# Kernel tuning notes

Hardware: AMD Instinct MI355X
Metric: run time of the kernel (lower is better)

## Reference

```python
import jax, jax.numpy as jnp
import numpy as np

K = 3          # kernel_size
G = 8          # groups
R = 4          # channel reduction ratio
D = 1          # dilation
M = D * (K - 1)
M2 = M // 2


def setup_inputs() -> dict:
    key = jax.random.key(0)
    ks = jax.random.split(key, 5)
    B, C, Hin, Win = 8, 128, 130, 130
    Cr = C // R
    x = jax.random.normal(ks[0], (B, C, Hin, Win), jnp.float32)
    W_reduce = jax.random.normal(ks[1], (Cr, C), jnp.float32) / np.float32(np.sqrt(C))
    b_reduce = jax.random.normal(ks[2], (Cr,), jnp.float32) * 0.01
    W_kern = jax.random.normal(ks[3], (G * K * K, Cr), jnp.float32) / np.float32(np.sqrt(Cr))
    b_kern = jax.random.normal(ks[4], (G * K * K,), jnp.float32) * 0.01
    return dict(x=x, W_reduce=W_reduce, b_reduce=b_reduce, W_kern=W_kern, b_kern=b_kern)


def reference(x, W_reduce, b_reduce, W_kern, b_kern):
    B, C, Hin, Win = x.shape
    H, W = Hin - M, Win - M            # stride=1, padding=0
    CG = C // G
    # unfold (im2col), torch ordering: channel outer, kernel-position inner
    patches = jnp.stack(
        [x[:, :, i * D:i * D + H, j * D:j * D + W] for i in range(K) for j in range(K)],
        axis=2,
    )                                   # [B, C, K2, H, W]
    patches = patches.reshape(B, G, CG, K * K, H, W)
    # center crop for kernel generation (pool is Identity since stride=1)
    xc = x[:, :, M2:Hin - M2, M2:Win - M2]            # [B, C, H, W]
    red = jnp.einsum('rc,bchw->brhw', W_reduce, xc) + b_reduce[None, :, None, None]
    kern = jnp.einsum('or,brhw->bohw', W_kern, red) + b_kern[None, :, None, None]
    kern = kern.reshape(B, G, K * K, H, W)
    # per-pixel dynamic kernel multiply-sum over K2
    out = jnp.einsum('bgkhw,bgckhw->bgchw', kern, patches)
    return out.reshape(B, C, H, W)
```

## Files before the change

kernel.cpp:

```cpp
#include <hip/hip_runtime.h>

namespace {
constexpr int HIN = 130, WIN = 130;
constexpr int HH = 128, WW = 128;
constexpr int C = 128, CR = 32, B = 8;
constexpr int CHW = HIN * WIN;

__global__ void transpose_wred(const float* __restrict__ Wred, float* __restrict__ WredT) {
    int idx = blockIdx.x * 256 + threadIdx.x;
    int r = idx >> 7;
    int c = idx & 127;
    WredT[c * CR + r] = Wred[r * C + c];
}

__device__ __forceinline__ void lgkm_barrier() {
    asm volatile("s_waitcnt lgkmcnt(0)\n\ts_barrier" ::: "memory");
    __builtin_amdgcn_sched_barrier(0);
}

__global__ __launch_bounds__(256, 4) void invol_direct(
    const float* __restrict__ x,
    const float* __restrict__ WredT,
    const float* __restrict__ bred,
    const float* __restrict__ Wkern,
    const float* __restrict__ bkern,
    float* __restrict__ out)
{
    __shared__ float red2[CR][128];

    const int t = threadIdx.x;
    const int p = t & 63;
    const int q = __builtin_amdgcn_readfirstlane(t >> 6);

    const int orig = blockIdx.x;
    const int blk  = (orig & 7) * 128 + (orig >> 3);
    const int b    = blk >> 7;
    const int h    = blk & (HH - 1);

    const float* xb = x + (size_t)b * C * CHW;

    const float* xc = xb + (size_t)(h + 1) * WIN + (2 * p + 1);
    float r0[8], r1[8];
#pragma unroll
    for (int r = 0; r < 8; ++r) { r0[r] = bred[q * 8 + r]; r1[r] = r0[r]; }

#pragma unroll
    for (int cb = 0; cb < 4; ++cb) {
        float xv0[32], xv1[32];
#pragma unroll
        for (int cc = 0; cc < 32; ++cc) {
            const float* cp = xc + (size_t)(cb * 32 + cc) * CHW;
            xv0[cc] = cp[0];
            xv1[cc] = cp[1];
        }
#pragma unroll
        for (int cc = 0; cc < 32; ++cc) {
#pragma unroll
            for (int r = 0; r < 8; ++r) {
                float wgt = WredT[(cb * 32 + cc) * CR + q * 8 + r];
                r0[r] = fmaf(wgt, xv0[cc], r0[r]);
                r1[r] = fmaf(wgt, xv1[cc], r1[r]);
            }
        }
    }
#pragma unroll
    for (int r = 0; r < 8; ++r)
        *(float2*)&red2[q * 8 + r][2 * p] = make_float2(r0[r], r1[r]);

    lgkm_barrier();

    float k0[18], k1[18];
#pragma unroll
    for (int k = 0; k < 18; ++k) { k0[k] = bkern[18 * q + k]; k1[k] = k0[k]; }
#pragma unroll
    for (int r = 0; r < CR; ++r) {
        float2 rv = *(const float2*)&red2[r][2 * p];
#pragma unroll
        for (int k = 0; k < 18; ++k) {
            float wgt = Wkern[(18 * q + k) * CR + r];
            k0[k] = fmaf(wgt, rv.x, k0[k]);
            k1[k] = fmaf(wgt, rv.y, k1[k]);
        }
    }

    const float* xrow = xb + (size_t)h * WIN + 2 * p;
    float* op = out + (((size_t)(b * C + 32 * q)) * HH + h) * WW + 2 * p;

#pragma unroll
    for (int half = 0; half < 2; ++half) {
        float kh0[9], kh1[9];
#pragma unroll
        for (int k = 0; k < 9; ++k) { kh0[k] = k0[9 * half + k]; kh1[k] = k1[9 * half + k]; }

#pragma unroll 2
        for (int cc = 0; cc < 16; ++cc) {
            const float* xp = xrow + (size_t)(32 * q + 16 * half + cc) * CHW;
            float2 ta[3], tb[3];
#pragma unroll
            for (int i = 0; i < 3; ++i) {
                ta[i] = *(const float2*)(xp + i * WIN);
                tb[i] = *(const float2*)(xp + i * WIN + 2);
            }
            float a0 = 0.f, a1 = 0.f;
#pragma unroll
            for (int i = 0; i < 3; ++i) {
                a0 = fmaf(kh0[3 * i + 0], ta[i].x, a0);
                a0 = fmaf(kh0[3 * i + 1], ta[i].y, a0);
                a0 = fmaf(kh0[3 * i + 2], tb[i].x, a0);
                a1 = fmaf(kh1[3 * i + 0], ta[i].y, a1);
                a1 = fmaf(kh1[3 * i + 1], tb[i].x, a1);
                a1 = fmaf(kh1[3 * i + 2], tb[i].y, a1);
            }
            *(float2*)(op + (size_t)(16 * half + cc) * HH * WW) = make_float2(a0, a1);
        }
    }
}
}

extern "C" void kernel_launch(void* const* d_in, const int* in_sizes, int n_in,
                              void* d_out, int out_size, void* d_ws, size_t ws_size,
                              hipStream_t stream) {
    const float* x     = (const float*)d_in[0];
    const float* Wred  = (const float*)d_in[1];
    const float* bred  = (const float*)d_in[2];
    const float* Wkern = (const float*)d_in[3];
    const float* bkern = (const float*)d_in[4];
    float* out   = (float*)d_out;
    float* WredT = (float*)d_ws;

    transpose_wred<<<16, 256, 0, stream>>>(Wred, WredT);

    invol_direct<<<1024, 256, 0, stream>>>(x, WredT, bred, Wkern, bkern, out);
}
```

Measured before the change: 58.59 us.

## Software-pipeline channel loads with double buffers and compute kernel weights per half

Splits the channel-reduction loads into 16-channel chunks held in two register buffers, so the next chunk's global loads are issued before the FMAs on the current chunk. The output stage now prefetches the 3x3 patches of the next four channels while computing the current four. The first patch load is issued before the barrier. Kernel weights are generated one half (9 taps) at a time, interleaved with the output loop, which lowers the live register count. The risk is extra VGPR pressure from the 48 float2 patch buffers, which could hurt occupancy under launch_bounds(256,4) or cause spills.

```diff
diff --git a/kernel.cpp b/kernel.cpp
--- a/kernel.cpp
+++ b/kernel.cpp
@@ -44,76 +44,106 @@
 #pragma unroll
     for (int r = 0; r < 8; ++r) { r0[r] = bred[q * 8 + r]; r1[r] = r0[r]; }
 
+    float A0[16], A1[16], B0[16], B1[16];
+
+    auto ld1 = [&](float (&v0)[16], float (&v1)[16], int cb) {
 #pragma unroll
-    for (int cb = 0; cb < 4; ++cb) {
-        float xv0[32], xv1[32];
+        for (int cc = 0; cc < 16; ++cc) {
+            const float* cp = xc + (size_t)(cb * 16 + cc) * CHW;
+            v0[cc] = cp[0];
+            v1[cc] = cp[1];
+        }
+    };
+    auto fma1 = [&](const float (&v0)[16], const float (&v1)[16], int cb) {
 #pragma unroll
-        for (int cc = 0; cc < 32; ++cc) {
-            const float* cp = xc + (size_t)(cb * 32 + cc) * CHW;
-            xv0[cc] = cp[0];
-            xv1[cc] = cp[1];
-        }
-#pragma unroll
-        for (int cc = 0; cc < 32; ++cc) {
+        for (int cc = 0; cc < 16; ++cc) {
 #pragma unroll
             for (int r = 0; r < 8; ++r) {
-                float wgt = WredT[(cb * 32 + cc) * CR + q * 8 + r];
-                r0[r] = fmaf(wgt, xv0[cc], r0[r]);
-                r1[r] = fmaf(wgt, xv1[cc], r1[r]);
+                float wgt = WredT[(cb * 16 + cc) * CR + q * 8 + r];
+                r0[r] = fmaf(wgt, v0[cc], r0[r]);
+                r1[r] = fmaf(wgt, v1[cc], r1[r]);
             }
+        }
+    };
+
+    ld1(A0, A1, 0);
+#pragma unroll
+    for (int cb = 0; cb < 8; ++cb) {
+        if ((cb & 1) == 0) {
+            if (cb < 7) ld1(B0, B1, cb + 1);
+            fma1(A0, A1, cb);
+        } else {
+            if (cb < 7) ld1(A0, A1, cb + 1);
+            fma1(B0, B1, cb);
         }
     }
 #pragma unroll
     for (int r = 0; r < 8; ++r)
         *(float2*)&red2[q * 8 + r][2 * p] = make_float2(r0[r], r1[r]);
 
-    lgkm_barrier();
-
-    float k0[18], k1[18];
-#pragma unroll
-    for (int k = 0; k < 18; ++k) { k0[k] = bkern[18 * q + k]; k1[k] = k0[k]; }
-#pragma unroll
-    for (int r = 0; r < CR; ++r) {
-        float2 rv = *(const float2*)&red2[r][2 * p];
-#pragma unroll
-        for (int k = 0; k < 18; ++k) {
-            float wgt = Wkern[(18 * q + k) * CR + r];
-            k0[k] = fmaf(wgt, rv.x, k0[k]);
-            k1[k] = fmaf(wgt, rv.y, k1[k]);
-        }
-    }
-
     const float* xrow = xb + (size_t)h * WIN + 2 * p;
     float* op = out + (((size_t)(b * C + 32 * q)) * HH + h) * WW + 2 * p;
 
+    float2 TA[24], TB[24];
+
+    auto ldc = [&](float2 (&T)[24], int c0) {
 #pragma unroll
-    for (int half = 0; half < 2; ++half) {
-        float kh0[9], kh1[9];
-#pragma unroll
-        for (int k = 0; k < 9; ++k) { kh0[k] = k0[9 * half + k]; kh1[k] = k1[9 * half + k]; }
-
-#pragma unroll 2
-        for (int cc = 0; cc < 16; ++cc) {
-            const float* xp = xrow + (size_t)(32 * q + 16 * half + cc) * CHW;
-            float2 ta[3], tb[3];
+        for (int m = 0; m < 4; ++m) {
+            const float* xp = xrow + (size_t)(32 * q + c0 + m) * CHW;
 #pragma unroll
             for (int i = 0; i < 3; ++i) {
-                ta[i] = *(const float2*)(xp + i * WIN);
-                tb[i] = *(const float2*)(xp + i * WIN + 2);
+                T[6 * m + 2 * i]     = *(const float2*)(xp + i * WIN);
+                T[6 * m + 2 * i + 1] = *(const float2*)(xp + i * WIN + 2);
             }
+        }
+    };
+    float kh0[9], kh1[9];
+    auto kernhalf = [&](int half) {
+#pragma unroll
+        for (int k = 0; k < 9; ++k) { kh0[k] = bkern[18 * q + 9 * half + k]; kh1[k] = kh0[k]; }
+#pragma unroll
+        for (int r = 0; r < CR; ++r) {
+            float2 rv = *(const float2*)&red2[r][2 * p];
+#pragma unroll
+            for (int k = 0; k < 9; ++k) {
+                float wgt = Wkern[(18 * q + 9 * half + k) * CR + r];
+                kh0[k] = fmaf(wgt, rv.x, kh0[k]);
+                kh1[k] = fmaf(wgt, rv.y, kh1[k]);
+            }
+        }
+    };
+    auto fmac = [&](const float2 (&T)[24], int c0) {
+#pragma unroll
+        for (int m = 0; m < 4; ++m) {
             float a0 = 0.f, a1 = 0.f;
 #pragma unroll
             for (int i = 0; i < 3; ++i) {
-                a0 = fmaf(kh0[3 * i + 0], ta[i].x, a0);
-                a0 = fmaf(kh0[3 * i + 1], ta[i].y, a0);
-                a0 = fmaf(kh0[3 * i + 2], tb[i].x, a0);
-                a1 = fmaf(kh1[3 * i + 0], ta[i].y, a1);
-                a1 = fmaf(kh1[3 * i + 1], tb[i].x, a1);
-                a1 = fmaf(kh1[3 * i + 2], tb[i].y, a1);
+                float2 ta = T[6 * m + 2 * i];
+                float2 tb = T[6 * m + 2 * i + 1];
+                a0 = fmaf(kh0[3 * i + 0], ta.x, a0);
+                a0 = fmaf(kh0[3 * i + 1], ta.y, a0);
+                a0 = fmaf(kh0[3 * i + 2], tb.x, a0);
+                a1 = fmaf(kh1[3 * i + 0], ta.y, a1);
+                a1 = fmaf(kh1[3 * i + 1], tb.x, a1);
+                a1 = fmaf(kh1[3 * i + 2], tb.y, a1);
             }
-            *(float2*)(op + (size_t)(16 * half + cc) * HH * WW) = make_float2(a0, a1);
+            *(float2*)(op + (size_t)(c0 + m) * HH * WW) = make_float2(a0, a1);
         }
-    }
+    };
+
+    ldc(TA, 0);
+    lgkm_barrier();
+
+    kernhalf(0);
+    ldc(TB, 4);  fmac(TA, 0);
+    ldc(TA, 8);  fmac(TB, 4);
+    ldc(TB, 12); fmac(TA, 8);
+    ldc(TA, 16); fmac(TB, 12);
+    kernhalf(1);
+    ldc(TB, 20); fmac(TA, 16);
+    ldc(TA, 24); fmac(TB, 20);
+    ldc(TB, 28); fmac(TA, 24);
+    fmac(TB, 28);
 }
 }
 
```

Result: slower. 121.0 us (+106.6%).

## Software-pipeline involution loads with triple-buffered registers and split kernel generation

Applied to the files above, without the earlier changes.

Replaces the per-channel load-then-compute loop with a manual three-buffer register pipeline. Global loads for the next channel pair are issued before the FMAs for the current pair, and the first loads start before the LDS barrier. Kernel-weight generation is split into two halves, with the second half computed mid-pipeline, so only 18 kernel values are live at a time. The goal is to hide global load latency, at the cost of more registers for the 36 float2 tile buffers, which could reduce occupancy under launch_bounds(256,4).

```diff
diff --git a/kernel.cpp b/kernel.cpp
--- a/kernel.cpp
+++ b/kernel.cpp
@@ -67,53 +67,77 @@
     for (int r = 0; r < 8; ++r)
         *(float2*)&red2[q * 8 + r][2 * p] = make_float2(r0[r], r1[r]);
 
-    lgkm_barrier();
-
-    float k0[18], k1[18];
-#pragma unroll
-    for (int k = 0; k < 18; ++k) { k0[k] = bkern[18 * q + k]; k1[k] = k0[k]; }
-#pragma unroll
-    for (int r = 0; r < CR; ++r) {
-        float2 rv = *(const float2*)&red2[r][2 * p];
-#pragma unroll
-        for (int k = 0; k < 18; ++k) {
-            float wgt = Wkern[(18 * q + k) * CR + r];
-            k0[k] = fmaf(wgt, rv.x, k0[k]);
-            k1[k] = fmaf(wgt, rv.y, k1[k]);
-        }
-    }
-
     const float* xrow = xb + (size_t)h * WIN + 2 * p;
     float* op = out + (((size_t)(b * C + 32 * q)) * HH + h) * WW + 2 * p;
 
+    float2 T0[12], T1[12], T2[12];
+
+    auto ldc = [&](float2 (&T)[12], int j) {
 #pragma unroll
-    for (int half = 0; half < 2; ++half) {
-        float kh0[9], kh1[9];
-#pragma unroll
-        for (int k = 0; k < 9; ++k) { kh0[k] = k0[9 * half + k]; kh1[k] = k1[9 * half + k]; }
-
-#pragma unroll 2
-        for (int cc = 0; cc < 16; ++cc) {
-            const float* xp = xrow + (size_t)(32 * q + 16 * half + cc) * CHW;
-            float2 ta[3], tb[3];
+        for (int m = 0; m < 2; ++m) {
+            const float* xp = xrow + (size_t)(32 * q + 2 * j + m) * CHW;
 #pragma unroll
             for (int i = 0; i < 3; ++i) {
-                ta[i] = *(const float2*)(xp + i * WIN);
-                tb[i] = *(const float2*)(xp + i * WIN + 2);
+                T[6 * m + 2 * i]     = *(const float2*)(xp + i * WIN);
+                T[6 * m + 2 * i + 1] = *(const float2*)(xp + i * WIN + 2);
             }
+        }
+    };
+    float khA[9], khB[9];
+    auto kernhalf = [&](int half) {
+#pragma unroll
+        for (int k = 0; k < 9; ++k) { khA[k] = bkern[18 * q + 9 * half + k]; khB[k] = khA[k]; }
+#pragma unroll
+        for (int r = 0; r < CR; ++r) {
+            float2 rv = *(const float2*)&red2[r][2 * p];
+#pragma unroll
+            for (int k = 0; k < 9; ++k) {
+                float wgt = Wkern[(18 * q + 9 * half + k) * CR + r];
+                khA[k] = fmaf(wgt, rv.x, khA[k]);
+                khB[k] = fmaf(wgt, rv.y, khB[k]);
+            }
+        }
+    };
+    auto fmac = [&](const float2 (&T)[12], int j) {
+#pragma unroll
+        for (int m = 0; m < 2; ++m) {
             float a0 = 0.f, a1 = 0.f;
 #pragma unroll
             for (int i = 0; i < 3; ++i) {
-                a0 = fmaf(kh0[3 * i + 0], ta[i].x, a0);
-                a0 = fmaf(kh0[3 * i + 1], ta[i].y, a0);
-                a0 = fmaf(kh0[3 * i + 2], tb[i].x, a0);
-                a1 = fmaf(kh1[3 * i + 0], ta[i].y, a1);
-                a1 = fmaf(kh1[3 * i + 1], tb[i].x, a1);
-                a1 = fmaf(kh1[3 * i + 2], tb[i].y, a1);
+                float2 ta = T[6 * m + 2 * i];
+                float2 tb = T[6 * m + 2 * i + 1];
+                a0 = fmaf(khA[3 * i + 0], ta.x, a0);
+                a0 = fmaf(khA[3 * i + 1], ta.y, a0);
+                a0 = fmaf(khA[3 * i + 2], tb.x, a0);
+                a1 = fmaf(khB[3 * i + 0], ta.y, a1);
+                a1 = fmaf(khB[3 * i + 1], tb.x, a1);
+                a1 = fmaf(khB[3 * i + 2], tb.y, a1);
             }
-            *(float2*)(op + (size_t)(16 * half + cc) * HH * WW) = make_float2(a0, a1);
+            *(float2*)(op + (size_t)(2 * j + m) * HH * WW) = make_float2(a0, a1);
         }
-    }
+    };
+
+    ldc(T0, 0); ldc(T1, 1);
+    lgkm_barrier();
+    kernhalf(0);
+
+    ldc(T2, 2);   fmac(T0, 0);
+    ldc(T0, 3);   fmac(T1, 1);
+    ldc(T1, 4);   fmac(T2, 2);
+    ldc(T2, 5);   fmac(T0, 3);
+    ldc(T0, 6);   fmac(T1, 4);
+    ldc(T1, 7);   fmac(T2, 5);
+    ldc(T2, 8);   fmac(T0, 6);
+    ldc(T0, 9);   fmac(T1, 7);
+    kernhalf(1);
+    ldc(T1, 10);  fmac(T2, 8);
+    ldc(T2, 11);  fmac(T0, 9);
+    ldc(T0, 12);  fmac(T1, 10);
+    ldc(T1, 13);  fmac(T2, 11);
+    ldc(T2, 14);  fmac(T0, 12);
+    ldc(T0, 15);  fmac(T1, 13);
+    fmac(T2, 14);
+    fmac(T0, 15);
 }
 }
 
```

New measurement: 74.55 us. 27.2% more time.

## Software-pipeline the involution tap loads with a triple register buffer

Applied to the files above, without the earlier changes.

Restructures the apply phase into a manually unrolled three-deep register pipeline. Each stage loads 3x3 windows for two channels while the FMAs for earlier channels run, and the first loads are issued before the LDS barrier so they overlap the kernel-generation step. Kernel weights are now produced one half (9 taps) at a time, which lowers live registers, and the occupancy hint in launch_bounds is dropped. The cost is 72 extra float registers for the buffers, which may still reduce occupancy, and the straight-line code is much larger.

```diff
diff --git a/kernel.cpp b/kernel.cpp
--- a/kernel.cpp
+++ b/kernel.cpp
@@ -18,7 +18,52 @@
     __builtin_amdgcn_sched_barrier(0);
 }
 
-__global__ __launch_bounds__(256, 4) void invol_direct(
+#define DECLBUF(T) float2 T##0, T##1, T##2, T##3, T##4, T##5, \
+                          T##6, T##7, T##8, T##9, T##10, T##11
+
+#define LDC(T, j) do { \
+    const float* xp_ = xrow + (size_t)(32 * q + 2 * (j)) * CHW; \
+    T##0 = *(const float2*)(xp_);            T##1 = *(const float2*)(xp_ + 2); \
+    T##2 = *(const float2*)(xp_ + WIN);      T##3 = *(const float2*)(xp_ + WIN + 2); \
+    T##4 = *(const float2*)(xp_ + 2 * WIN);  T##5 = *(const float2*)(xp_ + 2 * WIN + 2); \
+    const float* xq_ = xp_ + CHW; \
+    T##6 = *(const float2*)(xq_);            T##7 = *(const float2*)(xq_ + 2); \
+    T##8 = *(const float2*)(xq_ + WIN);      T##9 = *(const float2*)(xq_ + WIN + 2); \
+    T##10 = *(const float2*)(xq_ + 2 * WIN); T##11 = *(const float2*)(xq_ + 2 * WIN + 2); \
+} while (0)
+
+#define FMAC1(T, A, B, o0, o1, o2, o3, o4, o5, joff) do { \
+    float a0_ = 0.f, a1_ = 0.f; \
+    a0_ = fmaf(A[0], T##o0.x, a0_); a0_ = fmaf(A[1], T##o0.y, a0_); a0_ = fmaf(A[2], T##o1.x, a0_); \
+    a1_ = fmaf(B[0], T##o0.y, a1_); a1_ = fmaf(B[1], T##o1.x, a1_); a1_ = fmaf(B[2], T##o1.y, a1_); \
+    a0_ = fmaf(A[3], T##o2.x, a0_); a0_ = fmaf(A[4], T##o2.y, a0_); a0_ = fmaf(A[5], T##o3.x, a0_); \
+    a1_ = fmaf(B[3], T##o2.y, a1_); a1_ = fmaf(B[4], T##o3.x, a1_); a1_ = fmaf(B[5], T##o3.y, a1_); \
+    a0_ = fmaf(A[6], T##o4.x, a0_); a0_ = fmaf(A[7], T##o4.y, a0_); a0_ = fmaf(A[8], T##o5.x, a0_); \
+    a1_ = fmaf(B[6], T##o4.y, a1_); a1_ = fmaf(B[7], T##o5.x, a1_); a1_ = fmaf(B[8], T##o5.y, a1_); \
+    *(float2*)(op + (size_t)(joff) * HH * WW) = make_float2(a0_, a1_); \
+} while (0)
+
+#define FMAC(T, j) do { \
+    FMAC1(T, khA, khB, 0, 1, 2, 3, 4, 5, 2 * (j)); \
+    FMAC1(T, khA, khB, 6, 7, 8, 9, 10, 11, 2 * (j) + 1); \
+} while (0)
+
+#define KERNHALF(half) do { \
+    _Pragma("unroll") \
+    for (int k = 0; k < 9; ++k) { khA[k] = bkern[18 * q + 9 * (half) + k]; khB[k] = khA[k]; } \
+    _Pragma("unroll") \
+    for (int r = 0; r < CR; ++r) { \
+        float2 rv_ = *(const float2*)&red2[r][2 * p]; \
+        _Pragma("unroll") \
+        for (int k = 0; k < 9; ++k) { \
+            float wgt_ = Wkern[(18 * q + 9 * (half) + k) * CR + r]; \
+            khA[k] = fmaf(wgt_, rv_.x, khA[k]); \
+            khB[k] = fmaf(wgt_, rv_.y, khB[k]); \
+        } \
+    } \
+} while (0)
+
+__global__ __launch_bounds__(256) void invol_direct(
     const float* __restrict__ x,
     const float* __restrict__ WredT,
     const float* __restrict__ bred,
@@ -67,53 +112,33 @@
     for (int r = 0; r < 8; ++r)
         *(float2*)&red2[q * 8 + r][2 * p] = make_float2(r0[r], r1[r]);
 
-    lgkm_barrier();
-
-    float k0[18], k1[18];
-#pragma unroll
-    for (int k = 0; k < 18; ++k) { k0[k] = bkern[18 * q + k]; k1[k] = k0[k]; }
-#pragma unroll
-    for (int r = 0; r < CR; ++r) {
-        float2 rv = *(const float2*)&red2[r][2 * p];
-#pragma unroll
-        for (int k = 0; k < 18; ++k) {
-            float wgt = Wkern[(18 * q + k) * CR + r];
-            k0[k] = fmaf(wgt, rv.x, k0[k]);
-            k1[k] = fmaf(wgt, rv.y, k1[k]);
-        }
-    }
-
     const float* xrow = xb + (size_t)h * WIN + 2 * p;
     float* op = out + (((size_t)(b * C + 32 * q)) * HH + h) * WW + 2 * p;
 
-#pragma unroll
-    for (int half = 0; half < 2; ++half) {
-        float kh0[9], kh1[9];
-#pragma unroll
-        for (int k = 0; k < 9; ++k) { kh0[k] = k0[9 * half + k]; kh1[k] = k1[9 * half + k]; }
+    float khA[9], khB[9];
+    DECLBUF(U); DECLBUF(V); DECLBUF(W);
 
-#pragma unroll 2
-        for (int cc = 0; cc < 16; ++cc) {
-            const float* xp = xrow + (size_t)(32 * q + 16 * half + cc) * CHW;
-            float2 ta[3], tb[3];
-#pragma unroll
-            for (int i = 0; i < 3; ++i) {
-                ta[i] = *(const float2*)(xp + i * WIN);
-                tb[i] = *(const float2*)(xp + i * WIN + 2);
-            }
-            float a0 = 0.f, a1 = 0.f;
-#pragma unroll
-            for (int i = 0; i < 3; ++i) {
-                a0 = fmaf(kh0[3 * i + 0], ta[i].x, a0);
-                a0 = fmaf(kh0[3 * i + 1], ta[i].y, a0);
-                a0 = fmaf(kh0[3 * i + 2], tb[i].x, a0);
-                a1 = fmaf(kh1[3 * i + 0], ta[i].y, a1);
-                a1 = fmaf(kh1[3 * i + 1], tb[i].x, a1);
-                a1 = fmaf(kh1[3 * i + 2], tb[i].y, a1);
-            }
-            *(float2*)(op + (size_t)(16 * half + cc) * HH * WW) = make_float2(a0, a1);
-        }
-    }
+    LDC(U, 0); LDC(V, 1);
+    lgkm_barrier();
+    KERNHALF(0);
+
+    LDC(W, 2);   FMAC(U, 0);
+    LDC(U, 3);   FMAC(V, 1);
+    LDC(V, 4);   FMAC(W, 2);
+    LDC(W, 5);   FMAC(U, 3);
+    LDC(U, 6);   FMAC(V, 4);
+    LDC(V, 7);   FMAC(W, 5);
+    LDC(W, 8);   FMAC(U, 6);
+    LDC(U, 9);   FMAC(V, 7);
+    KERNHALF(1);
+    LDC(V, 10);  FMAC(W, 8);
+    LDC(W, 11);  FMAC(U, 9);
+    LDC(U, 12);  FMAC(V, 10);
+    LDC(V, 13);  FMAC(W, 11);
+    LDC(W, 14);  FMAC(U, 12);
+    LDC(U, 15);  FMAC(V, 13);
+    FMAC(W, 14);
+    FMAC(U, 15);
 }
 }
 
```

Measured after the change: 79.81 us. +36.2%, slower.
